# Optimization experiments

Hardware: AMD Instinct MI355X
Metric: run time of the kernel (lower is better)

The kernel has to match this reference:

```python
import jax, jax.numpy as jnp
import numpy as np

B_, S_, P_, D_ = 2, 512, 64, 1024
L_ = 4            # n_layer
DI_ = 2 * D_      # d_inner (expand=2)
DS_ = 16          # d_state
DC_ = 4           # d_conv
DR_ = D_ // 16    # dt_rank
PCD_ = 768        # prepend_cond_dim


def setup_inputs() -> dict:
    key = jax.random.key(0)
    ks = jax.random.split(key, 12)
    n = lambda k, s, sc=0.02: jax.random.normal(k, s, dtype=jnp.float32) * sc
    A_log = jnp.log(jnp.broadcast_to(jnp.arange(1, DS_ + 1, dtype=jnp.float32), (L_, DI_, DS_)))
    return {
        'x': jax.random.normal(ks[0], (B_, S_, D_), dtype=jnp.float32),
        'prepend_cond': jax.random.normal(ks[1], (B_, P_, PCD_), dtype=jnp.float32),
        'pre_w1': n(ks[2], (PCD_, D_)),
        'pre_w2': n(ks[3], (D_, D_)),
        'norm_w': jnp.ones((L_, D_), jnp.float32),
        'in_proj_w': n(ks[4], (L_, 2 * DI_, D_)),
        'conv_w': n(ks[5], (L_, DI_, DC_), 0.1),
        'conv_b': jnp.zeros((L_, DI_), jnp.float32),
        'x_proj_w': n(ks[6], (L_, DR_ + 2 * DS_, DI_)),
        'dt_proj_w': n(ks[7], (L_, DI_, DR_), 0.1),
        'dt_proj_b': jax.random.uniform(ks[8], (L_, DI_), jnp.float32, -4.0, -2.0),
        'A_log': A_log,
        'D_param': jnp.ones((L_, DI_), jnp.float32),
        'out_proj_w': n(ks[9], (L_, D_, DI_)),
        'final_norm_w': jnp.ones((D_,), jnp.float32),
    }


def rmsnorm(x, w, eps=1e-5):
    return x * jax.lax.rsqrt(jnp.mean(x * x, axis=-1, keepdims=True) + eps) * w


def mamba_block(x, ip_w, cw, cb, xp_w, dtp_w, dtp_b, A_log, Dp, op_w):
    B, S, _ = x.shape
    xz = jnp.einsum('bsd,ed->bse', x, ip_w)            # [B,S,2*DI]
    xi, z = jnp.split(xz, 2, axis=-1)
    # depthwise causal conv1d along time
    xt = xi.transpose(0, 2, 1)                          # [B,DI,S]
    conv = jax.lax.conv_general_dilated(
        xt, cw[:, None, :], (1,), [(DC_ - 1, 0)], feature_group_count=DI_) + cb[:, None]
    xi = jax.nn.silu(conv.transpose(0, 2, 1))           # [B,S,DI]
    xdbl = jnp.einsum('bse,fe->bsf', xi, xp_w)          # [B,S,DR+2*DS]
    dt, Bm, Cm = jnp.split(xdbl, [DR_, DR_ + DS_], axis=-1)
    dt = jax.nn.softplus(jnp.einsum('bsr,er->bse', dt, dtp_w) + dtp_b)  # [B,S,DI]
    A = -jnp.exp(A_log)                                 # [DI,DS]
    dA = jnp.exp(dt[..., None] * A)                     # [B,S,DI,DS]
    dBu = dt[..., None] * Bm[:, :, None, :] * xi[..., None]

    def step(h, t):
        da, dbu, c = t
        h = da * h + dbu                                # [B,DI,DS]
        return h, jnp.einsum('bes,bs->be', h, c)

    h0 = jnp.zeros((B, DI_, DS_), x.dtype)
    _, ys = jax.lax.scan(step, h0, (dA.transpose(1, 0, 2, 3), dBu.transpose(1, 0, 2, 3), Cm.transpose(1, 0, 2)))
    y = ys.transpose(1, 0, 2) + xi * Dp
    y = y * jax.nn.silu(z)
    return jnp.einsum('bse,de->bsd', y, op_w)


def reference(x, prepend_cond, pre_w1, pre_w2, norm_w, in_proj_w, conv_w, conv_b,
              x_proj_w, dt_proj_w, dt_proj_b, A_log, D_param, out_proj_w, final_norm_w):
    p = jax.nn.silu(prepend_cond @ pre_w1) @ pre_w2     # to_prepend_embed
    h = jnp.concatenate([p, x], axis=1)                 # [B, P+S, D]
    for l in range(L_):
        h = h + mamba_block(rmsnorm(h, norm_w[l]), in_proj_w[l], conv_w[l], conv_b[l],
                            x_proj_w[l], dt_proj_w[l], dt_proj_b[l], A_log[l],
                            D_param[l], out_proj_w[l])
    h = rmsnorm(h, final_norm_w)
    return h[:, P_:, :]
```

## Files before the change

### kernel.cpp

```cpp
#include <hip/hip_runtime.h>
#include <math.h>

#define B_ 2
#define S_ 512
#define P_ 64
#define T_ 576
#define D_ 1024
#define L_ 4
#define DI_ 2048
#define DS_ 16
#define DC_ 4
#define DR_ 64
#define PCD_ 768
#define M_ (B_*T_)
#define CCH 18
#define NC (T_/CCH)
#define XKS 16
#define OPK 4

#define N_IP (2*DI_*D_/4)
#define N_XP (96*DI_/4)
#define N_DTP (DI_*DR_/4)
#define N_OP (D_*DI_/4)
#define CVB ((N_IP + N_XP + N_DTP + N_OP + 255) / 256)
#define SETSZ ((size_t)2*DI_*D_ + 96*DI_ + DI_*DR_ + D_*DI_)

typedef __attribute__((ext_vector_type(8))) short bf16x8;
typedef __attribute__((ext_vector_type(4))) float f32x4;

__device__ __forceinline__ float silu_f(float v) { return v / (1.f + __expf(-v)); }
__device__ __forceinline__ float softplus_f(float v) {
    return fmaxf(v, 0.f) + log1pf(__expf(-fabsf(v)));
}
__device__ __forceinline__ unsigned short bf16_rne(float x) {
    unsigned int b = __float_as_uint(x);
    b += 0x7fffu + ((b >> 16) & 1u);
    return (unsigned short)(b >> 16);
}
__device__ __forceinline__ float bf16_to_f(unsigned short u) {
    return __uint_as_float((unsigned int)u << 16);
}

typedef const void __attribute__((address_space(1)))* gas_t;
typedef void __attribute__((address_space(3)))* las_t;
__device__ __forceinline__ void async16(const void* g, void* l) {
    __builtin_amdgcn_global_load_lds((gas_t)g, (las_t)l, 16, 0, 0);
}

__device__ __forceinline__ void cvt4_body(int i,
    const float* s0, unsigned short* d0, int n0,
    const float* s1, unsigned short* d1, int n1,
    const float* s2, unsigned short* d2, int n2,
    const float* s3, unsigned short* d3, int n3)
{
    const float* s; unsigned short* d; int off;
    if (i < n0)                     { s = s0; d = d0; off = i; }
    else if (i < n0 + n1)           { s = s1; d = d1; off = i - n0; }
    else if (i < n0 + n1 + n2)      { s = s2; d = d2; off = i - n0 - n1; }
    else if (i < n0 + n1 + n2 + n3) { s = s3; d = d3; off = i - n0 - n1 - n2; }
    else return;
    const float4 v = ((const float4*)s)[off];
    ushort4 o;
    o.x = bf16_rne(v.x); o.y = bf16_rne(v.y);
    o.z = bf16_rne(v.z); o.w = bf16_rne(v.w);
    ((ushort4*)d)[off] = o;
}

template<int EPI, int BN>
__global__ __launch_bounds__(256) void gemm_mfma_kernel(
    const unsigned short* __restrict__ A, const unsigned short* __restrict__ W,
    float* __restrict__ C, float* __restrict__ C2,
    int M, int N, int K, int Kchunk)
{
    constexpr int NF = BN / 32;
    __shared__ unsigned short As[2][128 * 32];
    __shared__ unsigned short Bs[2][BN * 32];
    const int tid = threadIdx.x;
    const int wave = tid >> 6;
    const int lane = tid & 63;
    const int m0 = blockIdx.y * 128, n0 = blockIdx.x * BN;
    const int kbase = blockIdx.z * Kchunk;
    const int wm = (wave >> 1) * 64, wn = (wave & 1) * (BN / 2);

    const int srow = (wave << 5) + (lane >> 2);
    const int selem = (lane & 3) * 8;
    const unsigned short* gA = A + (size_t)(m0 + srow) * K + kbase + selem;
    const unsigned short* gB = W + (size_t)(n0 + srow) * K + kbase + selem;
    const int lofs = (wave << 5) * 32;

    f32x4 acc[4][NF];
    #pragma unroll
    for (int i = 0; i < 4; ++i)
        #pragma unroll
        for (int j = 0; j < NF; ++j)
            acc[i][j] = (f32x4){0.f, 0.f, 0.f, 0.f};

    const int fr = lane & 15;
    const int fq = lane >> 4;
    const int aoff = (wm + fr) * 32 + fq * 8;
    const int boff = (wn + fr) * 32 + fq * 8;

    const int NT = Kchunk >> 5;

    #define STAGE(b, t) do {                                              \
        const unsigned short* pA = gA + (t) * 32;                         \
        async16(pA, &As[b][lofs]);                                        \
        async16(pA + (size_t)16 * K, &As[b][lofs + 16 * 32]);             \
        if (BN == 128 || wave < BN / 32) {                                \
            const unsigned short* pB = gB + (t) * 32;                     \
            async16(pB, &Bs[b][lofs]);                                    \
            async16(pB + (size_t)16 * K, &Bs[b][lofs + 16 * 32]);         \
        }                                                                 \
    } while (0)

    STAGE(0, 0);
    __syncthreads();
    for (int t = 0; t < NT; ++t) {
        const int cur = t & 1;
        if (t + 1 < NT) STAGE(cur ^ 1, t + 1);
        bf16x8 af[4], bf[NF];
        #pragma unroll
        for (int i = 0; i < 4; ++i) af[i] = *(const bf16x8*)&As[cur][aoff + i * 512];
        #pragma unroll
        for (int j = 0; j < NF; ++j) bf[j] = *(const bf16x8*)&Bs[cur][boff + j * 512];
        #pragma unroll
        for (int i = 0; i < 4; ++i)
            #pragma unroll
            for (int j = 0; j < NF; ++j)
                acc[i][j] = __builtin_amdgcn_mfma_f32_16x16x32_bf16(
                    af[i], bf[j], acc[i][j], 0, 0, 0);
        __syncthreads();
    }
    #undef STAGE

    #pragma unroll
    for (int i = 0; i < 4; ++i) {
        const int m = m0 + wm + i * 16 + fq * 4;
        #pragma unroll
        for (int j = 0; j < NF; ++j) {
            const int n = n0 + wn + j * 16 + fr;
            if (EPI == 6) {
                float* p = C + ((size_t)blockIdx.z * M + m) * N + n;
                #pragma unroll
                for (int r = 0; r < 4; ++r)
                    p[(size_t)r * N] = acc[i][j][r];
            } else if (EPI == 8) {
                unsigned short* p = (unsigned short*)C +
                                    ((size_t)blockIdx.z * M + m) * N + n;
                #pragma unroll
                for (int r = 0; r < 4; ++r)
                    p[(size_t)r * N] = bf16_rne(acc[i][j][r]);
            } else if (EPI == 7) {
                if (n < DI_) {
                    unsigned short* p = (unsigned short*)C + (size_t)m * DI_ + n;
                    #pragma unroll
                    for (int r = 0; r < 4; ++r)
                        p[(size_t)r * DI_] = bf16_rne(acc[i][j][r]);
                } else {
                    unsigned short* p = (unsigned short*)C2 + (size_t)m * DI_ + (n - DI_);
                    #pragma unroll
                    for (int r = 0; r < 4; ++r)
                        p[(size_t)r * DI_] = bf16_rne(silu_f(acc[i][j][r]));
                }
            }
        }
    }
}

__global__ __launch_bounds__(256) void xproj_mfma_kernel(
    const unsigned short* __restrict__ A,
    const unsigned short* __restrict__ W,
    float* __restrict__ P)
{
    __shared__ unsigned short As[2][128 * 32];
    __shared__ unsigned short Bs[2][96 * 32];
    const int tid = threadIdx.x;
    const int wave = tid >> 6;
    const int lane = tid & 63;
    const int m0 = blockIdx.y * 128;
    const int kbase = blockIdx.x * (DI_ / XKS);
    const int wm = (wave >> 1) * 64, wn = (wave & 1) * 48;

    const int srow = (wave << 5) + (lane >> 2);
    const int selem = (lane & 3) * 8;
    const unsigned short* gA = A + (size_t)(m0 + srow) * DI_ + kbase + selem;
    const unsigned short* gB = W + (size_t)srow * DI_ + kbase + selem;
    const int lofs = (wave << 5) * 32;

    f32x4 acc[4][3];
    #pragma unroll
    for (int i = 0; i < 4; ++i)
        #pragma unroll
        for (int j = 0; j < 3; ++j)
            acc[i][j] = (f32x4){0.f, 0.f, 0.f, 0.f};

    const int fr = lane & 15;
    const int fq = lane >> 4;
    const int aoff = (wm + fr) * 32 + fq * 8;
    const int boff = (wn + fr) * 32 + fq * 8;

    #define XSTAGE(b, t) do {                                             \
        const unsigned short* pA = gA + (t) * 32;                         \
        async16(pA, &As[b][lofs]);                                        \
        async16(pA + (size_t)16 * DI_, &As[b][lofs + 16 * 32]);           \
        if (wave < 3) {                                                   \
            const unsigned short* pB = gB + (t) * 32;                     \
            async16(pB, &Bs[b][lofs]);                                    \
            async16(pB + (size_t)16 * DI_, &Bs[b][lofs + 16 * 32]);       \
        }                                                                 \
    } while (0)

    XSTAGE(0, 0);
    __syncthreads();
    #pragma unroll
    for (int t = 0; t < 4; ++t) {
        const int cur = t & 1;
        if (t + 1 < 4) XSTAGE(cur ^ 1, t + 1);
        bf16x8 af[4], bf[3];
        #pragma unroll
        for (int i = 0; i < 4; ++i) af[i] = *(const bf16x8*)&As[cur][aoff + i * 512];
        #pragma unroll
        for (int j = 0; j < 3; ++j) bf[j] = *(const bf16x8*)&Bs[cur][boff + j * 512];
        #pragma unroll
        for (int i = 0; i < 4; ++i)
            #pragma unroll
            for (int j = 0; j < 3; ++j)
                acc[i][j] = __builtin_amdgcn_mfma_f32_16x16x32_bf16(
                    af[i], bf[j], acc[i][j], 0, 0, 0);
        __syncthreads();
    }
    #undef XSTAGE

    float* Pb = P + ((size_t)blockIdx.x * M_ + m0) * 96;
    #pragma unroll
    for (int i = 0; i < 4; ++i) {
        const int m = wm + i * 16 + fq * 4;
        #pragma unroll
        for (int j = 0; j < 3; ++j) {
            const int n = wn + j * 16 + fr;
            #pragma unroll
            for (int r = 0; r < 4; ++r)
                Pb[(size_t)(m + r) * 96 + n] = acc[i][j][r];
        }
    }
}

__global__ __launch_bounds__(256) void xproj_reduce_kernel(
    const float* __restrict__ P, float* __restrict__ Bc, float* __restrict__ Cc,
    unsigned short* __restrict__ dtr_bf)
{
    const int i = blockIdx.x * 256 + threadIdx.x;
    if (i >= M_ * 96) return;
    float s = 0.f;
    #pragma unroll
    for (int ks = 0; ks < XKS; ++ks) s += P[(size_t)ks * (M_ * 96) + i];
    const int m = i / 96;
    const int n = i - m * 96;
    if (n < DR_)            dtr_bf[(size_t)m * DR_ + n] = bf16_rne(s);
    else if (n < DR_ + DS_) Bc[(size_t)m * DS_ + (n - DR_)] = s;
    else                    Cc[(size_t)m * DS_ + (n - DR_ - DS_)] = s;
}

__global__ __launch_bounds__(256) void cvt_bf16_kernel(
    const float* __restrict__ in, unsigned short* __restrict__ out, int n4)
{
    const int i = blockIdx.x * 256 + threadIdx.x;
    if (i >= n4) return;
    const float4 v = ((const float4*)in)[i];
    ushort4 o;
    o.x = bf16_rne(v.x); o.y = bf16_rne(v.y);
    o.z = bf16_rne(v.z); o.w = bf16_rne(v.w);
    ((ushort4*)out)[i] = o;
}

__global__ __launch_bounds__(256) void cvt_transpose_kernel(
    const float* __restrict__ in, unsigned short* __restrict__ out, int K, int N)
{
    __shared__ float t[64][65];
    const int k0 = blockIdx.x * 64;
    const int n0 = blockIdx.y * 64;
    const int tx = threadIdx.x & 63;
    const int ty = threadIdx.x >> 6;
    #pragma unroll
    for (int j = 0; j < 16; ++j) {
        const int kk = ty * 16 + j;
        t[kk][tx] = in[(size_t)(k0 + kk) * N + n0 + tx];
    }
    __syncthreads();
    #pragma unroll
    for (int j = 0; j < 16; ++j) {
        const int nn = ty * 16 + j;
        out[(size_t)(n0 + nn) * K + k0 + tx] = bf16_rne(t[tx][nn]);
    }
}

__global__ __launch_bounds__(256) void reduce_silu_bf16_kernel(
    const float* __restrict__ P, unsigned short* __restrict__ o, int MN, int ns)
{
    const int i = blockIdx.x * 256 + threadIdx.x;
    if (i >= MN) return;
    float s = 0.f;
    for (int k = 0; k < ns; ++k) s += P[(size_t)k * MN + i];
    o[i] = bf16_rne(silu_f(s));
}
__global__ __launch_bounds__(256) void reduce_fp32_kernel(
    const float* __restrict__ P, float* __restrict__ o, int MN, int ns)
{
    const int i = blockIdx.x * 256 + threadIdx.x;
    if (i >= MN) return;
    float s = 0.f;
    for (int k = 0; k < ns; ++k) s += P[(size_t)k * MN + i];
    o[i] = s;
}

__global__ __launch_bounds__(256) void outproj_rmsnorm_cvt_kernel(
    const unsigned short* __restrict__ P, float* __restrict__ h,
    const float* __restrict__ w, unsigned short* __restrict__ outb, int donorm,
    const float* s0, unsigned short* d0, int n0,
    const float* s1, unsigned short* d1, int n1,
    const float* s2, unsigned short* d2, int n2,
    const float* s3, unsigned short* d3, int n3)
{
    const int bid = blockIdx.x;
    if (bid >= M_) {
        cvt4_body((bid - M_) * 256 + threadIdx.x,
                  s0, d0, n0, s1, d1, n1, s2, d2, n2, s3, d3, n3);
        return;
    }
    const int r = bid;
    const int i = r * 256 + threadIdx.x;
    float4 v = ((float4*)h)[i];
    #pragma unroll
    for (int k = 0; k < OPK; ++k) {
        const ushort4 a4 = ((const ushort4*)P)[(size_t)k * (M_ * D_ / 4) + i];
        v.x += bf16_to_f(a4.x); v.y += bf16_to_f(a4.y);
        v.z += bf16_to_f(a4.z); v.w += bf16_to_f(a4.w);
    }
    ((float4*)h)[i] = v;
    if (!donorm) return;
    float ss = v.x * v.x + v.y * v.y + v.z * v.z + v.w * v.w;
    ss += __shfl_xor(ss, 32, 64);
    ss += __shfl_xor(ss, 16, 64);
    ss += __shfl_xor(ss, 8, 64);
    ss += __shfl_xor(ss, 4, 64);
    ss += __shfl_xor(ss, 2, 64);
    ss += __shfl_xor(ss, 1, 64);
    __shared__ float red[4];
    if ((threadIdx.x & 63) == 0) red[threadIdx.x >> 6] = ss;
    __syncthreads();
    const float tot = red[0] + red[1] + red[2] + red[3];
    const float scale = rsqrtf(tot * (1.f / D_) + 1e-5f);
    const float4 wv = ((const float4*)w)[threadIdx.x];
    ushort4 o;
    o.x = bf16_rne(v.x * scale * wv.x);
    o.y = bf16_rne(v.y * scale * wv.y);
    o.z = bf16_rne(v.z * scale * wv.z);
    o.w = bf16_rne(v.w * scale * wv.w);
    ((ushort4*)(outb + (size_t)r * D_))[threadIdx.x] = o;
}

__global__ __launch_bounds__(256) void assemble_h_kernel(
    const float* __restrict__ p, const float* __restrict__ x, float* __restrict__ h)
{
    const int idx = blockIdx.x * 256 + threadIdx.x;
    const int r = idx >> 8;
    const int c = idx & 255;
    const int b = r / T_;
    const int t = r - b * T_;
    float4 v;
    if (t < P_) v = ((const float4*)p)[(size_t)(b * P_ + t) * 256 + c];
    else        v = ((const float4*)x)[(size_t)(b * S_ + (t - P_)) * 256 + c];
    ((float4*)h)[idx] = v;
}

__global__ __launch_bounds__(256) void rmsnorm_cvt_kernel(
    const float* __restrict__ x, const float* __restrict__ w,
    unsigned short* __restrict__ outb,
    const float* s0, unsigned short* d0, int n0,
    const float* s1, unsigned short* d1, int n1,
    const float* s2, unsigned short* d2, int n2,
    const float* s3, unsigned short* d3, int n3)
{
    const int bid = blockIdx.x;
    if (bid >= M_) {
        cvt4_body((bid - M_) * 256 + threadIdx.x,
                  s0, d0, n0, s1, d1, n1, s2, d2, n2, s3, d3, n3);
        return;
    }
    const int r = bid;
    const float4 v = ((const float4*)(x + (size_t)r * D_))[threadIdx.x];
    float ss = v.x * v.x + v.y * v.y + v.z * v.z + v.w * v.w;
    ss += __shfl_xor(ss, 32, 64);
    ss += __shfl_xor(ss, 16, 64);
    ss += __shfl_xor(ss, 8, 64);
    ss += __shfl_xor(ss, 4, 64);
    ss += __shfl_xor(ss, 2, 64);
    ss += __shfl_xor(ss, 1, 64);
    __shared__ float red[4];
    if ((threadIdx.x & 63) == 0) red[threadIdx.x >> 6] = ss;
    __syncthreads();
    const float tot = red[0] + red[1] + red[2] + red[3];
    const float scale = rsqrtf(tot * (1.f / D_) + 1e-5f);
    const float4 wv = ((const float4*)w)[threadIdx.x];
    ushort4 o;
    o.x = bf16_rne(v.x * scale * wv.x);
    o.y = bf16_rne(v.y * scale * wv.y);
    o.z = bf16_rne(v.z * scale * wv.z);
    o.w = bf16_rne(v.w * scale * wv.w);
    ((ushort4*)(outb + (size_t)r * D_))[threadIdx.x] = o;
}

__global__ __launch_bounds__(256) void final_rmsnorm_kernel(
    const float* __restrict__ h, const float* __restrict__ w, float* __restrict__ out)
{
    const int r = blockIdx.x;
    const int b = r / S_;
    const int s = r - b * S_;
    const int hr = b * T_ + P_ + s;
    const float4 v = ((const float4*)(h + (size_t)hr * D_))[threadIdx.x];
    float ss = v.x * v.x + v.y * v.y + v.z * v.z + v.w * v.w;
    ss += __shfl_xor(ss, 32, 64);
    ss += __shfl_xor(ss, 16, 64);
    ss += __shfl_xor(ss, 8, 64);
    ss += __shfl_xor(ss, 4, 64);
    ss += __shfl_xor(ss, 2, 64);
    ss += __shfl_xor(ss, 1, 64);
    __shared__ float red[4];
    if ((threadIdx.x & 63) == 0) red[threadIdx.x >> 6] = ss;
    __syncthreads();
    const float tot = red[0] + red[1] + red[2] + red[3];
    const float scale = rsqrtf(tot * (1.f / D_) + 1e-5f);
    const float4 wv = ((const float4*)w)[threadIdx.x];
    float4 o;
    o.x = v.x * scale * wv.x; o.y = v.y * scale * wv.y;
    o.z = v.z * scale * wv.z; o.w = v.w * scale * wv.w;
    ((float4*)(out + (size_t)r * D_))[threadIdx.x] = o;
}

__global__ __launch_bounds__(256) void conv_silu_kernel(
    const unsigned short* __restrict__ xb, const float* __restrict__ cw,
    const float* __restrict__ cb, unsigned short* __restrict__ xib)
{
    __shared__ float xs[67][64];
    const int tid = threadIdx.x;
    const int tx = tid & 63;
    const int ty = tid >> 6;
    const int r0 = blockIdx.x * 64;
    const int e0 = blockIdx.y * 64;
    const int bt0 = (r0 / T_) * T_;

    for (int j = ty; j < 67; j += 4) {
        const int r = r0 + j - 3;
        xs[j][tx] = (r >= bt0) ? bf16_to_f(xb[(size_t)r * DI_ + e0 + tx]) : 0.f;
    }
    __syncthreads();
    const float4 w = *(const float4*)(cw + (size_t)(e0 + tx) * 4);
    const float bias = cb[e0 + tx];
    #pragma unroll
    for (int j = 0; j < 16; ++j) {
        const int rl = ty * 16 + j;
        float v = bias;
        v = fmaf(w.x, xs[rl + 0][tx], v);
        v = fmaf(w.y, xs[rl + 1][tx], v);
        v = fmaf(w.z, xs[rl + 2][tx], v);
        v = fmaf(w.w, xs[rl + 3][tx], v);
        xib[(size_t)(r0 + rl) * DI_ + e0 + tx] = bf16_rne(silu_f(v));
    }
}

__global__ __launch_bounds__(256) void scan_chunk1_kernel(
    const unsigned short* __restrict__ dtr,
    const unsigned short* __restrict__ dtw,
    const float* __restrict__ dtbias,
    const float* __restrict__ Bc,
    const unsigned short* __restrict__ xib,
    const float* __restrict__ A_log,
    float* __restrict__ Ap, float* __restrict__ Hp)
{
    __shared__ float4 Bs[CCH][4];
    __shared__ float dtrs[CCH][DR_];
    const int tid = threadIdx.x;
    const int e = ((blockIdx.x & 7) << 8) + tid;
    const int cb = blockIdx.x >> 3;
    const int b = cb & (B_ - 1);
    const int c = cb >> 1;
    const int r0 = b * T_ + c * CCH;
    for (int i = tid; i < CCH * DS_; i += 256)
        ((float*)Bs)[i] = Bc[(size_t)r0 * DS_ + i];
    for (int i = tid; i < CCH * DR_ / 4; i += 256) {
        const ushort4 v4 = ((const ushort4*)(dtr + (size_t)r0 * DR_))[i];
        float* d = &dtrs[0][0] + i * 4;
        d[0] = bf16_to_f(v4.x); d[1] = bf16_to_f(v4.y);
        d[2] = bf16_to_f(v4.z); d[3] = bf16_to_f(v4.w);
    }
    float A2[DS_], h[DS_], a[DS_];
    const float* Ae = A_log + (size_t)e * DS_;
    #pragma unroll
    for (int s = 0; s < DS_; ++s) {
        A2[s] = -__expf(Ae[s]) * 1.44269504f;
        h[s] = 0.f; a[s] = 1.f;
    }
    __syncthreads();
    float dt[CCH];
    {
        float w[DR_];
        const ushort4* wp = (const ushort4*)(dtw + (size_t)e * DR_);
        #pragma unroll
        for (int q = 0; q < 16; ++q) {
            const ushort4 v = wp[q];
            w[q * 4 + 0] = bf16_to_f(v.x);
            w[q * 4 + 1] = bf16_to_f(v.y);
            w[q * 4 + 2] = bf16_to_f(v.z);
            w[q * 4 + 3] = bf16_to_f(v.w);
        }
        const float bb = dtbias[e];
        #pragma unroll
        for (int t = 0; t < CCH; ++t) {
            float acc = 0.f;
            #pragma unroll
            for (int r = 0; r < DR_; ++r) acc = fmaf(dtrs[t][r], w[r], acc);
            dt[t] = softplus_f(acc + bb);
        }
    }
    const unsigned short* up = xib + (size_t)r0 * DI_ + e;
    #pragma unroll
    for (int t = 0; t < CCH; ++t) {
        const float dtv = dt[t];
        const float dtu = dtv * bf16_to_f(up[(size_t)t * DI_]);
        #pragma unroll
        for (int q = 0; q < 4; ++q) {
            const float4 bq = Bs[t][q];
            const float* bb = &bq.x;
            #pragma unroll
            for (int j = 0; j < 4; ++j) {
                const int s = q * 4 + j;
                const float da = __builtin_amdgcn_exp2f(dtv * A2[s]);
                a[s] *= da;
                h[s] = fmaf(da, h[s], bb[j] * dtu);
            }
        }
    }
    const size_t o = (size_t)cb * DS_ * DI_ + e;
    #pragma unroll
    for (int s = 0; s < DS_; ++s) {
        Ap[o + (size_t)s * DI_] = a[s];
        Hp[o + (size_t)s * DI_] = h[s];
    }
}

__global__ __launch_bounds__(256) void scan_chunk2_kernel(
    float* __restrict__ Ap, float* __restrict__ Hp)
{
    const int g = blockIdx.x * 256 + threadIdx.x;
    float h = 0.f;
    #pragma unroll
    for (int c = 0; c < NC; ++c) {
        const size_t o = (size_t)c * (B_ * DI_ * DS_) + g;
        const float ap = Ap[o];
        const float hp = Hp[o];
        Hp[o] = h;
        h = fmaf(ap, h, hp);
    }
}

__global__ __launch_bounds__(256) void scan_chunk3_kernel(
    const unsigned short* __restrict__ dtr,
    const unsigned short* __restrict__ dtw,
    const float* __restrict__ dtbias,
    const float* __restrict__ Bc,
    const float* __restrict__ Cc,
    const unsigned short* __restrict__ xib,
    const unsigned short* __restrict__ szb,
    const float* __restrict__ A_log, const float* __restrict__ Dp,
    const float* __restrict__ Hin, unsigned short* __restrict__ y)
{
    __shared__ float4 Bs[CCH][4], Cs[CCH][4];
    __shared__ float dtrs[CCH][DR_];
    const int tid = threadIdx.x;
    const int e = ((blockIdx.x & 7) << 8) + tid;
    const int cb = blockIdx.x >> 3;
    const int b = cb & (B_ - 1);
    const int c = cb >> 1;
    const int r0 = b * T_ + c * CCH;
    for (int i = tid; i < CCH * DS_; i += 256) {
        ((float*)Bs)[i] = Bc[(size_t)r0 * DS_ + i];
        ((float*)Cs)[i] = Cc[(size_t)r0 * DS_ + i];
    }
    for (int i = tid; i < CCH * DR_ / 4; i += 256) {
        const ushort4 v4 = ((const ushort4*)(dtr + (size_t)r0 * DR_))[i];
        float* d = &dtrs[0][0] + i * 4;
        d[0] = bf16_to_f(v4.x); d[1] = bf16_to_f(v4.y);
        d[2] = bf16_to_f(v4.z); d[3] = bf16_to_f(v4.w);
    }
    float A2[DS_], h[DS_];
    const float* Ae = A_log + (size_t)e * DS_;
    const float dpe = Dp[e];
    const size_t ho = (size_t)cb * DS_ * DI_ + e;
    #pragma unroll
    for (int s = 0; s < DS_; ++s) {
        A2[s] = -__expf(Ae[s]) * 1.44269504f;
        h[s] = Hin[ho + (size_t)s * DI_];
    }
    __syncthreads();
    float dt[CCH];
    {
        float w[DR_];
        const ushort4* wp = (const ushort4*)(dtw + (size_t)e * DR_);
        #pragma unroll
        for (int q = 0; q < 16; ++q) {
            const ushort4 v = wp[q];
            w[q * 4 + 0] = bf16_to_f(v.x);
            w[q * 4 + 1] = bf16_to_f(v.y);
            w[q * 4 + 2] = bf16_to_f(v.z);
            w[q * 4 + 3] = bf16_to_f(v.w);
        }
        const float bb = dtbias[e];
        #pragma unroll
        for (int t = 0; t < CCH; ++t) {
            float acc = 0.f;
            #pragma unroll
            for (int r = 0; r < DR_; ++r) acc = fmaf(dtrs[t][r], w[r], acc);
            dt[t] = softplus_f(acc + bb);
        }
    }
    const unsigned short* up = xib + (size_t)r0 * DI_ + e;
    const unsigned short* sp = szb + (size_t)r0 * DI_ + e;
    unsigned short* yp = y + (size_t)r0 * DI_ + e;
    #pragma unroll
    for (int t = 0; t < CCH; ++t) {
        const float dtv = dt[t];
        const float u   = bf16_to_f(up[(size_t)t * DI_]);
        const float dtu = dtv * u;
        float y0 = 0.f, y1 = 0.f, y2 = 0.f, y3 = 0.f;
        #pragma unroll
        for (int q = 0; q < 4; ++q) {
            const float4 bq = Bs[t][q];
            const float4 cq = Cs[t][q];
            const float* bb = &bq.x;
            const float* cc = &cq.x;
            #pragma unroll
            for (int j = 0; j < 4; ++j) {
                const int s = q * 4 + j;
                const float da = __builtin_amdgcn_exp2f(dtv * A2[s]);
                h[s] = fmaf(da, h[s], bb[j] * dtu);
                if (j == 0)      y0 = fmaf(h[s], cc[j], y0);
                else if (j == 1) y1 = fmaf(h[s], cc[j], y1);
                else if (j == 2) y2 = fmaf(h[s], cc[j], y2);
                else             y3 = fmaf(h[s], cc[j], y3);
            }
        }
        const float ysum = (y0 + y1) + (y2 + y3);
        const float yv = fmaf(u, dpe, ysum) * bf16_to_f(sp[(size_t)t * DI_]);
        yp[(size_t)t * DI_] = bf16_rne(yv);
    }
}

extern "C" void kernel_launch(void* const* d_in, const int* in_sizes, int n_in,
                              void* d_out, int out_size, void* d_ws, size_t ws_size,
                              hipStream_t stream)
{
    const float* x       = (const float*)d_in[0];
    const float* pc      = (const float*)d_in[1];
    const float* pre_w1  = (const float*)d_in[2];
    const float* pre_w2  = (const float*)d_in[3];
    const float* norm_w  = (const float*)d_in[4];
    const float* ip_w    = (const float*)d_in[5];
    const float* conv_w  = (const float*)d_in[6];
    const float* conv_b  = (const float*)d_in[7];
    const float* xp_w    = (const float*)d_in[8];
    const float* dtp_w   = (const float*)d_in[9];
    const float* dtp_b   = (const float*)d_in[10];
    const float* A_log   = (const float*)d_in[11];
    const float* D_param = (const float*)d_in[12];
    const float* op_w    = (const float*)d_in[13];
    const float* fnw     = (const float*)d_in[14];
    float* out = (float*)d_out;

    float* ws = (float*)d_ws;
    float* h    = ws;  ws += (size_t)M_ * D_;
    float* xz   = ws;  ws += (size_t)M_ * 2 * DI_;
    float* scr  = ws;  ws += (size_t)M_ * DI_;
    float* Pbuf = ws;  ws += (size_t)XKS * M_ * 96;
    float* Bc   = ws;  ws += (size_t)DS_ * M_;
    float* Cc   = ws;  ws += (size_t)DS_ * M_;
    unsigned short* xn_bf  = (unsigned short*)ws;  ws += (size_t)M_ * D_ / 2;
    unsigned short* yb_bf  = (unsigned short*)ws;  ws += (size_t)M_ * DI_ / 2;
    unsigned short* xi_bf  = (unsigned short*)ws;  ws += (size_t)M_ * DI_ / 2;
    unsigned short* xb_bf  = (unsigned short*)ws;  ws += (size_t)M_ * DI_ / 2;
    unsigned short* szb_bf = (unsigned short*)ws;  ws += (size_t)M_ * DI_ / 2;
    unsigned short* dtr_bf = (unsigned short*)ws;  ws += (size_t)M_ * DR_ / 2;
    unsigned short* wsets  = (unsigned short*)ws;  ws += SETSZ;
    ws += SETSZ;

    unsigned short* ipw_b[2], *xpw_b[2], *dtpw_b[2], *opw_b[2];
    for (int s = 0; s < 2; ++s) {
        unsigned short* base = wsets + (size_t)s * SETSZ;
        ipw_b[s]  = base;
        xpw_b[s]  = base + (size_t)2 * DI_ * D_;
        dtpw_b[s] = xpw_b[s] + (size_t)96 * DI_;
        opw_b[s]  = dtpw_b[s] + (size_t)DI_ * DR_;
    }

    float* Ap = xz;
    float* Hp = xz + (size_t)NC * B_ * DI_ * DS_;

    unsigned short* pc_bf   = xi_bf;
    unsigned short* w1t_bf  = ipw_b[0];
    unsigned short* w2t_bf  = ipw_b[0] + (size_t)D_ * PCD_;
    unsigned short* tmp1_bf = xn_bf;
    float*          tmp2    = Pbuf;
    float*          P2buf   = scr;
    unsigned short* Pop     = (unsigned short*)xz;

    const dim3 blk(256);

    cvt_bf16_kernel<<<dim3(B_ * P_ * PCD_ / 4 / 256), blk, 0, stream>>>(
        pc, pc_bf, B_ * P_ * PCD_ / 4);
    cvt_transpose_kernel<<<dim3(PCD_ / 64, D_ / 64), blk, 0, stream>>>(
        pre_w1, w1t_bf, PCD_, D_);
    cvt_transpose_kernel<<<dim3(D_ / 64, D_ / 64), blk, 0, stream>>>(
        pre_w2, w2t_bf, D_, D_);
    gemm_mfma_kernel<6, 64><<<dim3(D_ / 64, 1, 12), blk, 0, stream>>>(
        pc_bf, w1t_bf, Pbuf, nullptr, B_ * P_, D_, PCD_, PCD_ / 12);
    reduce_silu_bf16_kernel<<<dim3(B_ * P_ * D_ / 256), blk, 0, stream>>>(
        Pbuf, tmp1_bf, B_ * P_ * D_, 12);
    gemm_mfma_kernel<6, 64><<<dim3(D_ / 64, 1, 16), blk, 0, stream>>>(
        tmp1_bf, w2t_bf, P2buf, nullptr, B_ * P_, D_, D_, D_ / 16);
    reduce_fp32_kernel<<<dim3(B_ * P_ * D_ / 256), blk, 0, stream>>>(
        P2buf, tmp2, B_ * P_ * D_, 16);
    assemble_h_kernel<<<dim3(M_ * D_ / 4 / 256), blk, 0, stream>>>(tmp2, x, h);

    rmsnorm_cvt_kernel<<<dim3(M_ + CVB), blk, 0, stream>>>(
        h, norm_w, xn_bf,
        ip_w, ipw_b[0], N_IP,
        xp_w, xpw_b[0], N_XP,
        dtp_w, dtpw_b[0], N_DTP,
        op_w, opw_b[0], N_OP);

    for (int l = 0; l < L_; ++l) {
        const int s = l & 1;
        gemm_mfma_kernel<7, 64><<<dim3(2 * DI_ / 64, M_ / 128, 1), blk, 0, stream>>>(
            xn_bf, ipw_b[s], (float*)xb_bf, (float*)szb_bf, M_, 2 * DI_, D_, D_);
        conv_silu_kernel<<<dim3(M_ / 64, DI_ / 64), blk, 0, stream>>>(
            xb_bf, conv_w + (size_t)l * DI_ * DC_, conv_b + (size_t)l * DI_,
            xi_bf);
        xproj_mfma_kernel<<<dim3(XKS, M_ / 128), blk, 0, stream>>>(
            xi_bf, xpw_b[s], Pbuf);
        xproj_reduce_kernel<<<dim3((M_ * 96 + 255) / 256), blk, 0, stream>>>(
            Pbuf, Bc, Cc, dtr_bf);
        scan_chunk1_kernel<<<dim3(NC * B_ * DI_ / 256), blk, 0, stream>>>(
            dtr_bf, dtpw_b[s], dtp_b + (size_t)l * DI_, Bc, xi_bf,
            A_log + (size_t)l * DI_ * DS_, Ap, Hp);
        scan_chunk2_kernel<<<dim3(B_ * DI_ * DS_ / 256), blk, 0, stream>>>(Ap, Hp);
        scan_chunk3_kernel<<<dim3(NC * B_ * DI_ / 256), blk, 0, stream>>>(
            dtr_bf, dtpw_b[s], dtp_b + (size_t)l * DI_, Bc, Cc, xi_bf, szb_bf,
            A_log + (size_t)l * DI_ * DS_, D_param + (size_t)l * DI_, Hp, yb_bf);
        gemm_mfma_kernel<8, 64><<<dim3(D_ / 64, M_ / 128, OPK), blk, 0, stream>>>(
            yb_bf, opw_b[s], (float*)Pop, nullptr, M_, D_, DI_, DI_ / OPK);
        const int docvt = (l + 1 < L_);
        outproj_rmsnorm_cvt_kernel<<<dim3(M_ + (docvt ? CVB : 0)), blk, 0, stream>>>(
            Pop, h, norm_w + (size_t)((l + 1) & 3) * D_, xn_bf, l < L_ - 1,
            ip_w + (size_t)(l + 1) * 2 * DI_ * D_, ipw_b[s ^ 1], docvt ? N_IP : 0,
            xp_w + (size_t)(l + 1) * 96 * DI_, xpw_b[s ^ 1], docvt ? N_XP : 0,
            dtp_w + (size_t)(l + 1) * DI_ * DR_, dtpw_b[s ^ 1], docvt ? N_DTP : 0,
            op_w + (size_t)(l + 1) * D_ * DI_, opw_b[s ^ 1], docvt ? N_OP : 0);
    }

    final_rmsnorm_kernel<<<dim3(B_ * S_), blk, 0, stream>>>(h, fnw, out);
}
```

Baseline: 667.1 us.

## Convert fp32 in/out-proj weights to bf16 inside the GEMM load path

The in_proj and out_proj GEMMs now read fp32 weights straight from global memory, round them to bf16 in registers and write them into shared memory. This replaces the separate conversion pass that wrote a bf16 weight copy each layer. The three prepend conversion kernels are also merged into one launch. The trade-off is that the GEMMs read twice the weight bytes, with synchronous register loads instead of async LDS copies, and each weight tile is re-read and re-converted by every M-block.

```diff
diff --git a/kernel.cpp b/kernel.cpp
--- a/kernel.cpp
+++ b/kernel.cpp
@@ -18,12 +18,10 @@
 #define XKS 16
 #define OPK 4
 
-#define N_IP (2*DI_*D_/4)
 #define N_XP (96*DI_/4)
 #define N_DTP (DI_*DR_/4)
-#define N_OP (D_*DI_/4)
-#define CVB ((N_IP + N_XP + N_DTP + N_OP + 255) / 256)
-#define SETSZ ((size_t)2*DI_*D_ + 96*DI_ + DI_*DR_ + D_*DI_)
+#define CVB ((N_XP + N_DTP + 255) / 256)
+#define SETSZ ((size_t)96*DI_ + DI_*DR_)
 
 typedef __attribute__((ext_vector_type(8))) short bf16x8;
 typedef __attribute__((ext_vector_type(4))) float f32x4;
@@ -47,17 +45,13 @@
     __builtin_amdgcn_global_load_lds((gas_t)g, (las_t)l, 16, 0, 0);
 }
 
-__device__ __forceinline__ void cvt4_body(int i,
+__device__ __forceinline__ void cvt2_body(int i,
     const float* s0, unsigned short* d0, int n0,
-    const float* s1, unsigned short* d1, int n1,
-    const float* s2, unsigned short* d2, int n2,
-    const float* s3, unsigned short* d3, int n3)
+    const float* s1, unsigned short* d1, int n1)
 {
     const float* s; unsigned short* d; int off;
-    if (i < n0)                     { s = s0; d = d0; off = i; }
-    else if (i < n0 + n1)           { s = s1; d = d1; off = i - n0; }
-    else if (i < n0 + n1 + n2)      { s = s2; d = d2; off = i - n0 - n1; }
-    else if (i < n0 + n1 + n2 + n3) { s = s3; d = d3; off = i - n0 - n1 - n2; }
+    if (i < n0)           { s = s0; d = d0; off = i; }
+    else if (i < n0 + n1) { s = s1; d = d1; off = i - n0; }
     else return;
     const float4 v = ((const float4*)s)[off];
     ushort4 o;
@@ -66,9 +60,9 @@
     ((ushort4*)d)[off] = o;
 }
 
-template<int EPI, int BN>
+template<int EPI, int BN, bool WF32>
 __global__ __launch_bounds__(256) void gemm_mfma_kernel(
-    const unsigned short* __restrict__ A, const unsigned short* __restrict__ W,
+    const unsigned short* __restrict__ A, const void* __restrict__ Wv,
     float* __restrict__ C, float* __restrict__ C2,
     int M, int N, int K, int Kchunk)
 {
@@ -85,7 +79,12 @@
     const int srow = (wave << 5) + (lane >> 2);
     const int selem = (lane & 3) * 8;
     const unsigned short* gA = A + (size_t)(m0 + srow) * K + kbase + selem;
-    const unsigned short* gB = W + (size_t)(n0 + srow) * K + kbase + selem;
+    const unsigned short* gB16 = WF32 ? nullptr :
+        (const unsigned short*)Wv + (size_t)(n0 + srow) * K + kbase + selem;
+    const int brow = tid >> 2;
+    const int bke  = (tid & 3) * 8;
+    const float* gBw = WF32 ?
+        (const float*)Wv + (size_t)(n0 + brow) * K + kbase + bke : nullptr;
     const int lofs = (wave << 5) * 32;
 
     f32x4 acc[4][NF];
@@ -102,22 +101,43 @@
 
     const int NT = Kchunk >> 5;
 
-    #define STAGE(b, t) do {                                              \
+    #define STAGE_A(b, t) do {                                            \
         const unsigned short* pA = gA + (t) * 32;                         \
         async16(pA, &As[b][lofs]);                                        \
         async16(pA + (size_t)16 * K, &As[b][lofs + 16 * 32]);             \
-        if (BN == 128 || wave < BN / 32) {                                \
-            const unsigned short* pB = gB + (t) * 32;                     \
+    } while (0)
+    #define STAGE_B16(b, t) do {                                          \
+        if (wave < BN / 32) {                                             \
+            const unsigned short* pB = gB16 + (t) * 32;                   \
             async16(pB, &Bs[b][lofs]);                                    \
             async16(pB + (size_t)16 * K, &Bs[b][lofs + 16 * 32]);         \
         }                                                                 \
     } while (0)
-
-    STAGE(0, 0);
+    #define BW_WRITE(b) do {                                              \
+        bf16x8 pk;                                                        \
+        pk[0] = (short)bf16_rne(b0.x); pk[1] = (short)bf16_rne(b0.y);     \
+        pk[2] = (short)bf16_rne(b0.z); pk[3] = (short)bf16_rne(b0.w);     \
+        pk[4] = (short)bf16_rne(b1.x); pk[5] = (short)bf16_rne(b1.y);     \
+        pk[6] = (short)bf16_rne(b1.z); pk[7] = (short)bf16_rne(b1.w);     \
+        *(bf16x8*)&Bs[b][brow * 32 + bke] = pk;                           \
+    } while (0)
+
+    float4 b0, b1;
+    if (WF32) { b0 = *(const float4*)gBw; b1 = *(const float4*)(gBw + 4); }
+    STAGE_A(0, 0);
+    if (!WF32) STAGE_B16(0, 0);
+    if (WF32) BW_WRITE(0);
     __syncthreads();
     for (int t = 0; t < NT; ++t) {
         const int cur = t & 1;
-        if (t + 1 < NT) STAGE(cur ^ 1, t + 1);
+        if (t + 1 < NT) {
+            if (WF32) {
+                b0 = *(const float4*)(gBw + (size_t)(t + 1) * 32);
+                b1 = *(const float4*)(gBw + (size_t)(t + 1) * 32 + 4);
+            }
+            STAGE_A(cur ^ 1, t + 1);
+            if (!WF32) STAGE_B16(cur ^ 1, t + 1);
+        }
         bf16x8 af[4], bf[NF];
         #pragma unroll
         for (int i = 0; i < 4; ++i) af[i] = *(const bf16x8*)&As[cur][aoff + i * 512];
@@ -129,9 +149,12 @@
             for (int j = 0; j < NF; ++j)
                 acc[i][j] = __builtin_amdgcn_mfma_f32_16x16x32_bf16(
                     af[i], bf[j], acc[i][j], 0, 0, 0);
+        if (WF32 && t + 1 < NT) BW_WRITE(cur ^ 1);
         __syncthreads();
     }
-    #undef STAGE
+    #undef STAGE_A
+    #undef STAGE_B16
+    #undef BW_WRITE
 
     #pragma unroll
     for (int i = 0; i < 4; ++i) {
@@ -261,26 +284,34 @@
     else                    Cc[(size_t)m * DS_ + (n - DR_ - DS_)] = s;
 }
 
-__global__ __launch_bounds__(256) void cvt_bf16_kernel(
-    const float* __restrict__ in, unsigned short* __restrict__ out, int n4)
-{
-    const int i = blockIdx.x * 256 + threadIdx.x;
-    if (i >= n4) return;
-    const float4 v = ((const float4*)in)[i];
-    ushort4 o;
-    o.x = bf16_rne(v.x); o.y = bf16_rne(v.y);
-    o.z = bf16_rne(v.z); o.w = bf16_rne(v.w);
-    ((ushort4*)out)[i] = o;
-}
-
-__global__ __launch_bounds__(256) void cvt_transpose_kernel(
-    const float* __restrict__ in, unsigned short* __restrict__ out, int K, int N)
+__global__ __launch_bounds__(256) void prep_cvt_kernel(
+    const float* __restrict__ pc, unsigned short* __restrict__ pcb,
+    const float* __restrict__ w1, unsigned short* __restrict__ w1t,
+    const float* __restrict__ w2, unsigned short* __restrict__ w2t)
 {
     __shared__ float t[64][65];
-    const int k0 = blockIdx.x * 64;
-    const int n0 = blockIdx.y * 64;
+    const int bid = blockIdx.x;
     const int tx = threadIdx.x & 63;
     const int ty = threadIdx.x >> 6;
+    if (bid < 96) {
+        const int i = bid * 256 + threadIdx.x;
+        const float4 v = ((const float4*)pc)[i];
+        ushort4 o;
+        o.x = bf16_rne(v.x); o.y = bf16_rne(v.y);
+        o.z = bf16_rne(v.z); o.w = bf16_rne(v.w);
+        ((ushort4*)pcb)[i] = o;
+        return;
+    }
+    const float* in; unsigned short* outp; int K, N, k0, n0;
+    if (bid < 96 + 192) {
+        const int b = bid - 96;
+        K = PCD_; N = D_; in = w1; outp = w1t;
+        k0 = (b % (PCD_ / 64)) * 64; n0 = (b / (PCD_ / 64)) * 64;
+    } else {
+        const int b = bid - 288;
+        K = D_; N = D_; in = w2; outp = w2t;
+        k0 = (b % (D_ / 64)) * 64; n0 = (b / (D_ / 64)) * 64;
+    }
     #pragma unroll
     for (int j = 0; j < 16; ++j) {
         const int kk = ty * 16 + j;
@@ -290,7 +321,7 @@
     #pragma unroll
     for (int j = 0; j < 16; ++j) {
         const int nn = ty * 16 + j;
-        out[(size_t)(n0 + nn) * K + k0 + tx] = bf16_rne(t[tx][nn]);
+        outp[(size_t)(n0 + nn) * K + k0 + tx] = bf16_rne(t[tx][nn]);
     }
 }
 
@@ -317,14 +348,11 @@
     const unsigned short* __restrict__ P, float* __restrict__ h,
     const float* __restrict__ w, unsigned short* __restrict__ outb, int donorm,
     const float* s0, unsigned short* d0, int n0,
-    const float* s1, unsigned short* d1, int n1,
-    const float* s2, unsigned short* d2, int n2,
-    const float* s3, unsigned short* d3, int n3)
+    const float* s1, unsigned short* d1, int n1)
 {
     const int bid = blockIdx.x;
     if (bid >= M_) {
-        cvt4_body((bid - M_) * 256 + threadIdx.x,
-                  s0, d0, n0, s1, d1, n1, s2, d2, n2, s3, d3, n3);
+        cvt2_body((bid - M_) * 256 + threadIdx.x, s0, d0, n0, s1, d1, n1);
         return;
     }
     const int r = bid;
@@ -377,14 +405,11 @@
     const float* __restrict__ x, const float* __restrict__ w,
     unsigned short* __restrict__ outb,
     const float* s0, unsigned short* d0, int n0,
-    const float* s1, unsigned short* d1, int n1,
-    const float* s2, unsigned short* d2, int n2,
-    const float* s3, unsigned short* d3, int n3)
+    const float* s1, unsigned short* d1, int n1)
 {
     const int bid = blockIdx.x;
     if (bid >= M_) {
-        cvt4_body((bid - M_) * 256 + threadIdx.x,
-                  s0, d0, n0, s1, d1, n1, s2, d2, n2, s3, d3, n3);
+        cvt2_body((bid - M_) * 256 + threadIdx.x, s0, d0, n0, s1, d1, n1);
         return;
     }
     const int r = bid;
@@ -691,22 +716,21 @@
     unsigned short* dtr_bf = (unsigned short*)ws;  ws += (size_t)M_ * DR_ / 2;
     unsigned short* wsets  = (unsigned short*)ws;  ws += SETSZ;
     ws += SETSZ;
-
-    unsigned short* ipw_b[2], *xpw_b[2], *dtpw_b[2], *opw_b[2];
+    unsigned short* pw_bf  = (unsigned short*)ws;  ws += ((size_t)PCD_ * D_ + (size_t)D_ * D_ + 1) / 2;
+
+    unsigned short* xpw_b[2], *dtpw_b[2];
     for (int s = 0; s < 2; ++s) {
         unsigned short* base = wsets + (size_t)s * SETSZ;
-        ipw_b[s]  = base;
-        xpw_b[s]  = base + (size_t)2 * DI_ * D_;
-        dtpw_b[s] = xpw_b[s] + (size_t)96 * DI_;
-        opw_b[s]  = dtpw_b[s] + (size_t)DI_ * DR_;
+        xpw_b[s]  = base;
+        dtpw_b[s] = base + (size_t)96 * DI_;
     }
 
     float* Ap = xz;
     float* Hp = xz + (size_t)NC * B_ * DI_ * DS_;
 
     unsigned short* pc_bf   = xi_bf;
-    unsigned short* w1t_bf  = ipw_b[0];
-    unsigned short* w2t_bf  = ipw_b[0] + (size_t)D_ * PCD_;
+    unsigned short* w1t_bf  = pw_bf;
+    unsigned short* w2t_bf  = pw_bf + (size_t)D_ * PCD_;
     unsigned short* tmp1_bf = xn_bf;
     float*          tmp2    = Pbuf;
     float*          P2buf   = scr;
@@ -714,17 +738,13 @@
 
     const dim3 blk(256);
 
-    cvt_bf16_kernel<<<dim3(B_ * P_ * PCD_ / 4 / 256), blk, 0, stream>>>(
-        pc, pc_bf, B_ * P_ * PCD_ / 4);
-    cvt_transpose_kernel<<<dim3(PCD_ / 64, D_ / 64), blk, 0, stream>>>(
-        pre_w1, w1t_bf, PCD_, D_);
-    cvt_transpose_kernel<<<dim3(D_ / 64, D_ / 64), blk, 0, stream>>>(
-        pre_w2, w2t_bf, D_, D_);
-    gemm_mfma_kernel<6, 64><<<dim3(D_ / 64, 1, 12), blk, 0, stream>>>(
+    prep_cvt_kernel<<<dim3(96 + 192 + 256), blk, 0, stream>>>(
+        pc, pc_bf, pre_w1, w1t_bf, pre_w2, w2t_bf);
+    gemm_mfma_kernel<6, 64, false><<<dim3(D_ / 64, 1, 12), blk, 0, stream>>>(
         pc_bf, w1t_bf, Pbuf, nullptr, B_ * P_, D_, PCD_, PCD_ / 12);
     reduce_silu_bf16_kernel<<<dim3(B_ * P_ * D_ / 256), blk, 0, stream>>>(
         Pbuf, tmp1_bf, B_ * P_ * D_, 12);
-    gemm_mfma_kernel<6, 64><<<dim3(D_ / 64, 1, 16), blk, 0, stream>>>(
+    gemm_mfma_kernel<6, 64, false><<<dim3(D_ / 64, 1, 16), blk, 0, stream>>>(
         tmp1_bf, w2t_bf, P2buf, nullptr, B_ * P_, D_, D_, D_ / 16);
     reduce_fp32_kernel<<<dim3(B_ * P_ * D_ / 256), blk, 0, stream>>>(
         P2buf, tmp2, B_ * P_ * D_, 16);
@@ -732,15 +752,14 @@
 
     rmsnorm_cvt_kernel<<<dim3(M_ + CVB), blk, 0, stream>>>(
         h, norm_w, xn_bf,
-        ip_w, ipw_b[0], N_IP,
         xp_w, xpw_b[0], N_XP,
-        dtp_w, dtpw_b[0], N_DTP,
-        op_w, opw_b[0], N_OP);
+        dtp_w, dtpw_b[0], N_DTP);
 
     for (int l = 0; l < L_; ++l) {
         const int s = l & 1;
-        gemm_mfma_kernel<7, 64><<<dim3(2 * DI_ / 64, M_ / 128, 1), blk, 0, stream>>>(
-            xn_bf, ipw_b[s], (float*)xb_bf, (float*)szb_bf, M_, 2 * DI_, D_, D_);
+        gemm_mfma_kernel<7, 64, true><<<dim3(2 * DI_ / 64, M_ / 128, 1), blk, 0, stream>>>(
+            xn_bf, ip_w + (size_t)l * 2 * DI_ * D_,
+            (float*)xb_bf, (float*)szb_bf, M_, 2 * DI_, D_, D_);
         conv_silu_kernel<<<dim3(M_ / 64, DI_ / 64), blk, 0, stream>>>(
             xb_bf, conv_w + (size_t)l * DI_ * DC_, conv_b + (size_t)l * DI_,
             xi_bf);
@@ -755,15 +774,14 @@
         scan_chunk3_kernel<<<dim3(NC * B_ * DI_ / 256), blk, 0, stream>>>(
             dtr_bf, dtpw_b[s], dtp_b + (size_t)l * DI_, Bc, Cc, xi_bf, szb_bf,
             A_log + (size_t)l * DI_ * DS_, D_param + (size_t)l * DI_, Hp, yb_bf);
-        gemm_mfma_kernel<8, 64><<<dim3(D_ / 64, M_ / 128, OPK), blk, 0, stream>>>(
-            yb_bf, opw_b[s], (float*)Pop, nullptr, M_, D_, DI_, DI_ / OPK);
+        gemm_mfma_kernel<8, 64, true><<<dim3(D_ / 64, M_ / 128, OPK), blk, 0, stream>>>(
+            yb_bf, op_w + (size_t)l * D_ * DI_,
+            (float*)Pop, nullptr, M_, D_, DI_, DI_ / OPK);
         const int docvt = (l + 1 < L_);
         outproj_rmsnorm_cvt_kernel<<<dim3(M_ + (docvt ? CVB : 0)), blk, 0, stream>>>(
             Pop, h, norm_w + (size_t)((l + 1) & 3) * D_, xn_bf, l < L_ - 1,
-            ip_w + (size_t)(l + 1) * 2 * DI_ * D_, ipw_b[s ^ 1], docvt ? N_IP : 0,
             xp_w + (size_t)(l + 1) * 96 * DI_, xpw_b[s ^ 1], docvt ? N_XP : 0,
-            dtp_w + (size_t)(l + 1) * DI_ * DR_, dtpw_b[s ^ 1], docvt ? N_DTP : 0,
-            op_w + (size_t)(l + 1) * D_ * DI_, opw_b[s ^ 1], docvt ? N_OP : 0);
+            dtp_w + (size_t)(l + 1) * DI_ * DR_, dtpw_b[s ^ 1], docvt ? N_DTP : 0);
     }
 
     final_rmsnorm_kernel<<<dim3(B_ * S_), blk, 0, stream>>>(h, fnw, out);
```

New measurement: 710.0 us. 6.4% more time.
